# Optimization experiments

Measured on AMD Instinct MI355X. Metric: run time of the kernel, lower is better.

## Reference

```python
import jax, jax.numpy as jnp
import numpy as np

N_HEAD = 32
N_KV_HEAD = 8
HEAD_DIM = 64
N_EMBD = 2048
B, T = 2, 2048
ROPE_BASE = 10000.0


def _rope_cos_sin(T, head_dim, dtype):
    pos = jnp.arange(T, dtype=jnp.float32)
    dim_arr = jnp.arange(0, head_dim, 2, dtype=jnp.float32)
    freqs = ROPE_BASE ** (-dim_arr / head_dim)
    theta = jnp.outer(pos, freqs)                      # [T, hd/2]
    cos = jnp.concatenate([jnp.cos(theta), jnp.cos(theta)], axis=-1)  # [T, hd]
    sin = jnp.concatenate([jnp.sin(theta), jnp.sin(theta)], axis=-1)
    # broadcast to [1, T, 1, hd]
    return cos[None, :, None, :].astype(dtype), sin[None, :, None, :].astype(dtype)


def _rotate_half(v):
    h = v.shape[-1] // 2
    return jnp.concatenate([-v[..., h:], v[..., :h]], axis=-1)


def setup_inputs() -> dict:
    key = jax.random.key(0)
    kx, kq, kk, kv, ko = jax.random.split(key, 5)
    s = 1.0 / np.sqrt(N_EMBD)
    return {
        "x": jax.random.normal(kx, (B, T, N_EMBD), dtype=jnp.float32),
        "wq": jax.random.normal(kq, (N_EMBD, N_HEAD * HEAD_DIM), dtype=jnp.float32) * s,
        "wk": jax.random.normal(kk, (N_EMBD, N_KV_HEAD * HEAD_DIM), dtype=jnp.float32) * s,
        "wv": jax.random.normal(kv, (N_EMBD, N_KV_HEAD * HEAD_DIM), dtype=jnp.float32) * s,
        "wo": jax.random.normal(ko, (N_HEAD * HEAD_DIM, N_EMBD), dtype=jnp.float32) * s,
    }


def reference(x, wq, wk, wv, wo):
    Bx, Tx, C = x.shape
    n_rep = N_HEAD // N_KV_HEAD

    xq = (x @ wq).reshape(Bx, Tx, N_HEAD, HEAD_DIM)
    xk = (x @ wk).reshape(Bx, Tx, N_KV_HEAD, HEAD_DIM)
    xv = (x @ wv).reshape(Bx, Tx, N_KV_HEAD, HEAD_DIM)

    cos, sin = _rope_cos_sin(Tx, HEAD_DIM, x.dtype)
    xq = xq * cos + _rotate_half(xq) * sin
    xk = xk * cos + _rotate_half(xk) * sin

    # GQA: repeat_interleave KV heads to match query heads
    xk = jnp.repeat(xk, n_rep, axis=2)  # [B, T, H, hd]
    xv = jnp.repeat(xv, n_rep, axis=2)

    scale = 1.0 / np.sqrt(HEAD_DIM)
    # scores: [B, H, T, T]
    scores = jnp.einsum("bqhd,bkhd->bhqk", xq, xk) * scale
    causal = jnp.tril(jnp.ones((Tx, Tx), dtype=bool))
    scores = jnp.where(causal[None, None], scores, -jnp.inf)
    probs = jax.nn.softmax(scores, axis=-1)

    out = jnp.einsum("bhqk,bkhd->bqhd", probs, xv).reshape(Bx, Tx, N_HEAD * HEAD_DIM)
    return out @ wo
```

## Files before the change

### kernel.cpp

```cpp
#include <hip/hip_runtime.h>
#include <hip/hip_bf16.h>
#include <cstdint>
#include <cstddef>

#define B_ 2
#define T_ 2048
#define H_ 32
#define KVH_ 8
#define D_ 64
#define C_ 2048
#define NQKV 3072

typedef short short8 __attribute__((ext_vector_type(8)));
typedef float f32x4 __attribute__((ext_vector_type(4)));
typedef unsigned short u16;

__device__ __forceinline__ u16 f2b(float f) {
  union { float f; unsigned u; } x; x.f = f;
  unsigned r = x.u + 0x7fffu + ((x.u >> 16) & 1u);
  return (u16)(r >> 16);
}

__device__ __forceinline__ void gload16(const void* g, void* l) {
  __builtin_amdgcn_global_load_lds(
      (const __attribute__((address_space(1))) unsigned int*)g,
      (__attribute__((address_space(3))) unsigned int*)l,
      16, 0, 0);
}

__device__ __forceinline__ f32x4 mfma16(short8 a, short8 b, f32x4 c) {
  return __builtin_amdgcn_mfma_f32_16x16x32_bf16(a, b, c, 0, 0, 0);
}

__device__ __forceinline__ unsigned cvtpk(float lo_, float hi_) {
  unsigned r;
  asm("v_cvt_pk_bf16_f32 %0, %1, %2" : "=v"(r) : "v"(lo_), "v"(hi_));
  return r;
}

__global__ void k_tbl(float* __restrict__ tbl) {
  int i = blockIdx.x * 256 + threadIdx.x;
  int t = i >> 5, f = i & 31;
  double freq = pow(10000.0, -(double)f / 32.0);
  double th = (double)t * freq;
  tbl[i * 2 + 0] = (float)cos(th);
  tbl[i * 2 + 1] = (float)sin(th);
}

__global__ void k_cvtx(const float* __restrict__ x, u16* __restrict__ xb) {
  int i = blockIdx.x * 256 + threadIdx.x;
  float4 v = ((const float4*)x)[i];
  ushort4 o;
  o.x = f2b(v.x); o.y = f2b(v.y); o.z = f2b(v.z); o.w = f2b(v.w);
  ((ushort4*)xb)[i] = o;
}

__global__ void k_transw(const float* __restrict__ src, u16* __restrict__ dst, int N) {
  __shared__ float t[32][33];
  int tx = threadIdx.x, ty = threadIdx.y;
  int k0 = blockIdx.y * 32, n0 = blockIdx.x * 32;
#pragma unroll
  for (int i = 0; i < 4; i++)
    t[ty + i * 8][tx] = src[(size_t)(k0 + ty + i * 8) * N + n0 + tx];
  __syncthreads();
#pragma unroll
  for (int i = 0; i < 4; i++) {
    int nl = ty + i * 8;
    dst[(size_t)(n0 + nl) * 2048 + k0 + tx] = f2b(t[tx][nl]);
  }
}

template <int MODE>
__global__ __launch_bounds__(256, 2) void k_gemm(const u16* __restrict__ A,
                                                 const u16* __restrict__ Bt,
                                                 void* __restrict__ Cc,
                                                 int M, int N, int K,
                                                 const float* __restrict__ tbl,
                                                 u16* __restrict__ Qb,
                                                 u16* __restrict__ Kb,
                                                 u16* __restrict__ Vt) {
  __shared__ __align__(16) u16 As[128 * 64];
  __shared__ __align__(16) u16 Bs[128 * 64];
  const int tid = threadIdx.x;
  const int w = tid >> 6, l = tid & 63;
  const int lo = l & 15, hi = l >> 4;
  const int m0 = blockIdx.y * 128, n0 = blockIdx.x * 128;
  const int wr = w >> 1, wc = w & 1;
  f32x4 acc[4][4];
#pragma unroll
  for (int i = 0; i < 4; i++)
#pragma unroll
    for (int j = 0; j < 4; j++) acc[i][j] = (f32x4){0.f, 0.f, 0.f, 0.f};

  for (int k0 = 0; k0 < K; k0 += 64) {
#pragma unroll
    for (int i = 0; i < 4; i++) {
      int cid = i * 256 + tid;
      int row = cid >> 3, kc = cid & 7;
      gload16(A + (size_t)(m0 + row) * K + k0 + kc * 8, &As[(i * 256 + w * 64) * 8]);
      gload16(Bt + (size_t)(n0 + row) * K + k0 + kc * 8, &Bs[(i * 256 + w * 64) * 8]);
    }
    __syncthreads();
#pragma unroll
    for (int kk = 0; kk < 2; kk++) {
      short8 a[4], b[4];
#pragma unroll
      for (int i = 0; i < 4; i++)
        a[i] = *(const short8*)&As[(wr * 64 + i * 16 + lo) * 64 + kk * 32 + hi * 8];
#pragma unroll
      for (int j = 0; j < 4; j++)
        b[j] = *(const short8*)&Bs[(wc * 64 + j * 16 + lo) * 64 + kk * 32 + hi * 8];
#pragma unroll
      for (int i = 0; i < 4; i++)
#pragma unroll
        for (int j = 0; j < 4; j++) acc[i][j] = mfma16(a[i], b[j], acc[i][j]);
    }
    __syncthreads();
  }
  const int r0 = m0 + wr * 64, c0 = n0 + wc * 64;

  if (MODE == 0) {
#pragma unroll
    for (int i = 0; i < 4; i++)
#pragma unroll
      for (int j = 0; j < 4; j++) {
        f32x4 v = acc[i][j];
        int col = c0 + j * 16 + lo;
        int rw = r0 + i * 16 + hi * 4;
#pragma unroll
        for (int r = 0; r < 4; r++)
          ((float*)Cc)[(size_t)(rw + r) * N + col] = v[r];
      }
  } else {
    const int hd = c0 >> 6;
    const int b = m0 >> 11;
    if (hd < 40) {
      const bool isQ = (hd < 32);
      const float sc = isQ ? 0.125f * 1.44269504089f : 1.0f;
      u16* dst = isQ ? (Qb + (size_t)(b * H_ + hd) * T_ * 64)
                     : (Kb + (size_t)(b * KVH_ + (hd - 32)) * T_ * 64);
#pragma unroll
      for (int i = 0; i < 4; i++)
#pragma unroll
        for (int r = 0; r < 4; r++) {
          int t = (r0 + i * 16 + hi * 4 + r) & (T_ - 1);
          float2 cA = *(const float2*)&tbl[((size_t)t * 32 + lo) * 2];
          float2 cB = *(const float2*)&tbl[((size_t)t * 32 + 16 + lo) * 2];
          float a0 = acc[i][0][r], a1 = acc[i][1][r];
          float a2 = acc[i][2][r], a3 = acc[i][3][r];
          size_t rb = (size_t)t * 64;
          dst[rb + lo]      = f2b((a0 * cA.x - a2 * cA.y) * sc);
          dst[rb + 32 + lo] = f2b((a2 * cA.x + a0 * cA.y) * sc);
          dst[rb + 16 + lo] = f2b((a1 * cB.x - a3 * cB.y) * sc);
          dst[rb + 48 + lo] = f2b((a3 * cB.x + a1 * cB.y) * sc);
        }
    } else {
      const int kvh = hd - 40;
      u16* dst = Vt + (size_t)(b * KVH_ + kvh) * 64 * T_;
#pragma unroll
      for (int i = 0; i < 4; i++)
#pragma unroll
        for (int j = 0; j < 4; j++) {
          int t = (r0 + i * 16 + hi * 4) & (T_ - 1);
          int dd = j * 16 + lo;
          f32x4 v = acc[i][j];
          ushort4 ov;
          ov.x = f2b(v[0]); ov.y = f2b(v[1]); ov.z = f2b(v[2]); ov.w = f2b(v[3]);
          *(ushort4*)&dst[(size_t)dd * T_ + t] = ov;
        }
    }
  }
}

#define PSTR 40
__global__ __launch_bounds__(256)
__attribute__((amdgpu_waves_per_eu(3, 3)))
void k_attn(const u16* __restrict__ Qb,
            const u16* __restrict__ Kb,
            const u16* __restrict__ Vt,
            u16* __restrict__ Ob) {
  __shared__ __align__(16) u16 Pl[4][2][16 * PSTR];
  const int tid = threadIdx.x, w = tid >> 6, l = tid & 63;
  const int lo = l & 15, hi = l >> 4;
  const int b = blockIdx.z, h = blockIdx.y, kvh = h >> 2;
  const int p = (int)blockIdx.x * 4 + w;

  const size_t qbase = (size_t)(b * H_ + h) * T_ * 64;
  const size_t kbase = (size_t)(b * KVH_ + kvh) * T_ * 64;
  const size_t vbase = (size_t)(b * KVH_ + kvh) * 64 * T_;

  auto LOADK = [&](short8 (&ak)[2][2], int kv0) {
#pragma unroll
    for (int f = 0; f < 2; f++)
#pragma unroll
      for (int hf = 0; hf < 2; hf++)
        ak[f][hf] = *(const short8*)&Kb[kbase + (size_t)(kv0 + f * 16 + lo) * 64 + hf * 32 + hi * 8];
  };

  for (int pass = 0; pass < 2; pass++) {
    const int tile = pass ? (63 - p) : p;
    const int q0 = tile * 32;

    short8 aq[2][2];
#pragma unroll
    for (int qt = 0; qt < 2; qt++)
#pragma unroll
      for (int hf = 0; hf < 2; hf++)
        aq[qt][hf] = *(const short8*)&Qb[qbase + (size_t)(q0 + qt * 16 + lo) * 64 + hf * 32 + hi * 8];

    f32x4 o[2][4];
    float m[2], lsum[2];
#pragma unroll
    for (int qt = 0; qt < 2; qt++) {
      m[qt] = -1e30f; lsum[qt] = 0.f;
#pragma unroll
      for (int jd = 0; jd < 4; jd++) o[qt][jd] = (f32x4){0.f, 0.f, 0.f, 0.f};
    }

    auto STEP = [&](const short8 (&ak)[2][2], int kv0, bool masked) {
      short8 av[4];
#pragma unroll
      for (int jd = 0; jd < 4; jd++)
        av[jd] = *(const short8*)&Vt[vbase + (size_t)(jd * 16 + lo) * T_ + kv0 + hi * 8];

      f32x4 s[2][2];
      __builtin_amdgcn_s_setprio(1);
#pragma unroll
      for (int qt = 0; qt < 2; qt++)
#pragma unroll
        for (int f = 0; f < 2; f++) {
          f32x4 acc = (f32x4){0.f, 0.f, 0.f, 0.f};
          acc = mfma16(ak[f][0], aq[qt][0], acc);
          acc = mfma16(ak[f][1], aq[qt][1], acc);
          s[qt][f] = acc;
        }
      __builtin_amdgcn_s_setprio(0);

#pragma unroll
      for (int qt = 0; qt < 2; qt++) {
        const int myq = q0 + qt * 16 + lo;
        float p_[8];
#pragma unroll
        for (int f = 0; f < 2; f++)
#pragma unroll
          for (int r = 0; r < 4; r++) {
            float v = s[qt][f][r];
            if (masked) {
              int kv = kv0 + f * 16 + hi * 4 + r;
              v = (kv <= myq) ? v : -1e30f;
            }
            p_[f * 4 + r] = v;
          }
        float mx = fmaxf(fmaxf(fmaxf(p_[0], p_[1]), fmaxf(p_[2], p_[3])),
                         fmaxf(fmaxf(p_[4], p_[5]), fmaxf(p_[6], p_[7])));
        mx = fmaxf(mx, __shfl_xor(mx, 16));
        mx = fmaxf(mx, __shfl_xor(mx, 32));
        if (!__all(mx <= m[qt] + 11.5f)) {
          float mn = fmaxf(m[qt], mx);
          float a_ = exp2f(m[qt] - mn);
          m[qt] = mn;
          lsum[qt] *= a_;
#pragma unroll
          for (int jd = 0; jd < 4; jd++) {
            f32x4 t = o[qt][jd];
#pragma unroll
            for (int r = 0; r < 4; r++) t[r] *= a_;
            o[qt][jd] = t;
          }
        }
        float sm = 0.f;
#pragma unroll
        for (int i = 0; i < 8; i++) { p_[i] = exp2f(p_[i] - m[qt]); sm += p_[i]; }
        sm += __shfl_xor(sm, 16);
        sm += __shfl_xor(sm, 32);
        lsum[qt] += sm;
        uint2 w0, w1;
        w0.x = cvtpk(p_[0], p_[1]); w0.y = cvtpk(p_[2], p_[3]);
        w1.x = cvtpk(p_[4], p_[5]); w1.y = cvtpk(p_[6], p_[7]);
        *(uint2*)&Pl[w][qt][lo * PSTR + hi * 4] = w0;
        *(uint2*)&Pl[w][qt][lo * PSTR + 16 + hi * 4] = w1;
      }

#pragma unroll
      for (int qt = 0; qt < 2; qt++) {
        short8 pb = *(const short8*)&Pl[w][qt][lo * PSTR + hi * 8];
        __builtin_amdgcn_s_setprio(1);
#pragma unroll
        for (int jd = 0; jd < 4; jd++) o[qt][jd] = mfma16(av[jd], pb, o[qt][jd]);
        __builtin_amdgcn_s_setprio(0);
      }
    };

    short8 akA[2][2], akB[2][2];
    LOADK(akA, 0);
    int kv0 = 0;
    while (kv0 + 64 <= q0) {
      LOADK(akB, kv0 + 32);
      STEP(akA, kv0, false);
      LOADK(akA, kv0 + 64);
      STEP(akB, kv0 + 32, false);
      kv0 += 64;
    }
    if (kv0 < q0) {
      LOADK(akB, q0);
      STEP(akA, kv0, false);
      STEP(akB, q0, true);
    } else {
      STEP(akA, q0, true);
    }

#pragma unroll
    for (int qt = 0; qt < 2; qt++) {
      const int myq = q0 + qt * 16 + lo;
      float inv = 1.0f / lsum[qt];
      size_t obase = ((size_t)(b * T_ + myq) * H_ + h) * 64;
#pragma unroll
      for (int jd = 0; jd < 4; jd++) {
        ushort4 ov;
        ov.x = f2b(o[qt][jd][0] * inv);
        ov.y = f2b(o[qt][jd][1] * inv);
        ov.z = f2b(o[qt][jd][2] * inv);
        ov.w = f2b(o[qt][jd][3] * inv);
        *(ushort4*)&Ob[obase + jd * 16 + hi * 4] = ov;
      }
    }
  }
}

constexpr size_t OFF_TBL = 0;
constexpr size_t SZ_TBL = (size_t)T_ * 32 * 2 * 4;
constexpr size_t OFF_XB = OFF_TBL + SZ_TBL;
constexpr size_t SZ_XB = (size_t)B_ * T_ * C_ * 2;
constexpr size_t OFF_WQKVT = OFF_XB + SZ_XB;
constexpr size_t SZ_WQKVT = (size_t)NQKV * C_ * 2;
constexpr size_t OFF_WOT = OFF_WQKVT + SZ_WQKVT;
constexpr size_t SZ_WOT = (size_t)C_ * C_ * 2;
constexpr size_t OFF_QB = OFF_WOT + SZ_WOT;
constexpr size_t SZ_QB = (size_t)B_ * H_ * T_ * D_ * 2;
constexpr size_t OFF_KB = OFF_QB + SZ_QB;
constexpr size_t SZ_KVB = (size_t)B_ * KVH_ * T_ * D_ * 2;
constexpr size_t OFF_VT = OFF_KB + SZ_KVB;
constexpr size_t OFF_OB = OFF_VT + SZ_KVB;
constexpr size_t SZ_OB = (size_t)B_ * T_ * H_ * D_ * 2;

extern "C" void kernel_launch(void* const* d_in, const int* in_sizes, int n_in,
                              void* d_out, int out_size, void* d_ws, size_t ws_size,
                              hipStream_t stream) {
  const float* x = (const float*)d_in[0];
  const float* wq = (const float*)d_in[1];
  const float* wk = (const float*)d_in[2];
  const float* wv = (const float*)d_in[3];
  const float* wo = (const float*)d_in[4];

  char* ws = (char*)d_ws;
  float* tbl = (float*)(ws + OFF_TBL);
  u16* xb = (u16*)(ws + OFF_XB);
  u16* wqkvT = (u16*)(ws + OFF_WQKVT);
  u16* woT = (u16*)(ws + OFF_WOT);
  u16* Qb = (u16*)(ws + OFF_QB);
  u16* Kb = (u16*)(ws + OFF_KB);
  u16* Vt = (u16*)(ws + OFF_VT);
  u16* Ob = (u16*)(ws + OFF_OB);

  k_tbl<<<256, 256, 0, stream>>>(tbl);
  k_cvtx<<<8192, 256, 0, stream>>>(x, xb);
  dim3 tb(32, 8);
  k_transw<<<dim3(64, 64), tb, 0, stream>>>(wq, wqkvT, 2048);
  k_transw<<<dim3(16, 64), tb, 0, stream>>>(wk, wqkvT + (size_t)2048 * 2048, 512);
  k_transw<<<dim3(16, 64), tb, 0, stream>>>(wv, wqkvT + (size_t)2560 * 2048, 512);
  k_transw<<<dim3(64, 64), tb, 0, stream>>>(wo, woT, 2048);

  k_gemm<1><<<dim3(NQKV / 128, (B_ * T_) / 128), 256, 0, stream>>>(
      xb, wqkvT, nullptr, B_ * T_, NQKV, C_, tbl, Qb, Kb, Vt);
  k_attn<<<dim3(8, H_, B_), 256, 0, stream>>>(Qb, Kb, Vt, Ob);
  k_gemm<0><<<dim3(C_ / 128, (B_ * T_) / 128), 256, 0, stream>>>(
      Ob, woT, d_out, B_ * T_, C_, C_, nullptr, nullptr, nullptr, nullptr);
}
```

Measured before the change: 263.9 us.

## Software-pipeline QK MFMA of next tile with softmax of current tile

Splits the attention inner step into QK MFMA, softmax, and PV stages, and reorders the loop so the QK^T MFMAs for the next KV tile are issued between the current tile's softmax and its PV MFMAs. The goal is to overlap matrix-core work with the VALU exp/max work and hide latency. It adds a second score accumulator set, which raises register pressure, and replaces the unrolled two-step loop with a runtime useA branch that may cost some scheduling freedom.

```diff
diff --git a/kernel.cpp b/kernel.cpp
--- a/kernel.cpp
+++ b/kernel.cpp
@@ -217,13 +217,7 @@
       for (int jd = 0; jd < 4; jd++) o[qt][jd] = (f32x4){0.f, 0.f, 0.f, 0.f};
     }
 
-    auto STEP = [&](const short8 (&ak)[2][2], int kv0, bool masked) {
-      short8 av[4];
-#pragma unroll
-      for (int jd = 0; jd < 4; jd++)
-        av[jd] = *(const short8*)&Vt[vbase + (size_t)(jd * 16 + lo) * T_ + kv0 + hi * 8];
-
-      f32x4 s[2][2];
+    auto SMFMA = [&](const short8 (&ak)[2][2], f32x4 (&s)[2][2]) {
       __builtin_amdgcn_s_setprio(1);
 #pragma unroll
       for (int qt = 0; qt < 2; qt++)
@@ -235,7 +229,9 @@
           s[qt][f] = acc;
         }
       __builtin_amdgcn_s_setprio(0);
-
+    };
+
+    auto SOFTMAX = [&](const f32x4 (&s)[2][2], int kv0, bool masked) {
 #pragma unroll
       for (int qt = 0; qt < 2; qt++) {
         const int myq = q0 + qt * 16 + lo;
@@ -280,7 +276,9 @@
         *(uint2*)&Pl[w][qt][lo * PSTR + hi * 4] = w0;
         *(uint2*)&Pl[w][qt][lo * PSTR + 16 + hi * 4] = w1;
       }
-
+    };
+
+    auto PV = [&](const short8 (&av)[4]) {
 #pragma unroll
       for (int qt = 0; qt < 2; qt++) {
         short8 pb = *(const short8*)&Pl[w][qt][lo * PSTR + hi * 8];
@@ -291,22 +289,38 @@
       }
     };
 
+    auto LOADV = [&](short8 (&av)[4], int kv0) {
+#pragma unroll
+      for (int jd = 0; jd < 4; jd++)
+        av[jd] = *(const short8*)&Vt[vbase + (size_t)(jd * 16 + lo) * T_ + kv0 + hi * 8];
+    };
+
+    const int nsteps = (q0 >> 5) + 1;
     short8 akA[2][2], akB[2][2];
+    f32x4 sA[2][2], sB[2][2];
+    short8 av[4];
     LOADK(akA, 0);
+    SMFMA(akA, sA);
     int kv0 = 0;
-    while (kv0 + 64 <= q0) {
-      LOADK(akB, kv0 + 32);
-      STEP(akA, kv0, false);
-      LOADK(akA, kv0 + 64);
-      STEP(akB, kv0 + 32, false);
-      kv0 += 64;
-    }
-    if (kv0 < q0) {
-      LOADK(akB, q0);
-      STEP(akA, kv0, false);
-      STEP(akB, q0, true);
-    } else {
-      STEP(akA, q0, true);
+    bool useA = true;
+    for (int k = 0; k < nsteps; k++) {
+      const bool masked = (k == nsteps - 1);
+      const bool hasNext = !masked;
+      if (useA) {
+        if (hasNext) LOADK(akB, kv0 + 32);
+        LOADV(av, kv0);
+        SOFTMAX(sA, kv0, masked);
+        if (hasNext) SMFMA(akB, sB);
+        PV(av);
+      } else {
+        if (hasNext) LOADK(akA, kv0 + 32);
+        LOADV(av, kv0);
+        SOFTMAX(sB, kv0, masked);
+        if (hasNext) SMFMA(akA, sA);
+        PV(av);
+      }
+      kv0 += 32;
+      useA = !useA;
     }
 
 #pragma unroll
```

Measured after the change: 416.7 us. 57.9% more time.
